# Optimization experiments

Hardware: AMD Instinct MI355X
Metric: run time of the kernel (lower is better)

The kernel has to match this reference:

```python
import jax, jax.numpy as jnp
import numpy as np

NUM_NODES = 8192
NUM_EDGES = 262144
IN_C = 512
OUT_C = 512


def setup_inputs() -> dict:
    key = jax.random.key(0)
    k1, k2, k3, k4 = jax.random.split(key, 4)
    x = jax.random.normal(k1, (NUM_NODES, IN_C), dtype=jnp.float32)
    edge_index = jax.random.randint(k2, (2, NUM_EDGES), 0, NUM_NODES, dtype=jnp.int64)
    # nn.Linear params (W: [out, in], b: [out]) with kaiming-ish scale
    W = jax.random.normal(k3, (OUT_C, IN_C), dtype=jnp.float32) * (1.0 / np.sqrt(IN_C))
    b = jax.random.normal(k4, (OUT_C,), dtype=jnp.float32) * 0.01
    return {"x": x, "edge_index": edge_index, "W": W, "b": b}


def reference(x, edge_index, W, b):
    n = x.shape[0]
    # append self loops
    loop = jnp.arange(n, dtype=edge_index.dtype)
    rows = jnp.concatenate([edge_index[0], loop])
    cols = jnp.concatenate([edge_index[1], loop])
    # dense adjacency via scatter-set (duplicates collapse to 1.0, matching torch indexing assign)
    adj = jnp.zeros((n, n), dtype=jnp.float32).at[rows, cols].set(1.0)
    deg = adj.sum(axis=1)
    deg_inv_sqrt = jnp.where(deg > 0, jax.lax.rsqrt(jnp.maximum(deg, 1e-30)), 0.0)
    norm = deg_inv_sqrt[:, None] * adj * deg_inv_sqrt[None, :]
    h = x @ W.T + b            # [N, out_c]
    return norm @ h            # [N, out_c]
```

## Files before the change

### kernel.cpp

```cpp
#include <hip/hip_runtime.h>
#include <stdint.h>

#define N_NODES 8192
#define N_EDGES 262144
#define IN_C    512
#define OUT_C   512
#define MAX_DEG 128
#define X_ELEMS (N_NODES * IN_C)
#define W_ELEMS (OUT_C * IN_C)
#define BM_WORDS (N_NODES * (N_NODES / 32))

typedef __attribute__((ext_vector_type(8))) short short8;
typedef __attribute__((ext_vector_type(4))) float f32x4;

__device__ inline uint16_t f2bf(float f) {
    uint32_t u = __float_as_uint(f);
    uint32_t r = (u + 0x7FFFu + ((u >> 16) & 1u)) >> 16;
    return (uint16_t)r;
}

__global__ __launch_bounds__(256) void convert_k(const float* __restrict__ x,
                                                 const float* __restrict__ W,
                                                 uint16_t* __restrict__ xb,
                                                 uint16_t* __restrict__ wb,
                                                 int* __restrict__ cnt,
                                                 uint4* __restrict__ bm) {
    int tid = blockIdx.x * 256 + threadIdx.x;
    if (tid < N_NODES) cnt[tid] = 0;
    if (tid < BM_WORDS / 4) bm[tid] = make_uint4(0u, 0u, 0u, 0u);
    int i = tid * 8;
    const float* src; uint16_t* dst;
    if (i < X_ELEMS) { src = x + i; dst = xb + i; }
    else             { src = W + (i - X_ELEMS); dst = wb + (i - X_ELEMS); }
    float4 v0 = *(const float4*)(src);
    float4 v1 = *(const float4*)(src + 4);
    ushort4 o0, o1;
    o0.x = f2bf(v0.x); o0.y = f2bf(v0.y); o0.z = f2bf(v0.z); o0.w = f2bf(v0.w);
    o1.x = f2bf(v1.x); o1.y = f2bf(v1.y); o1.z = f2bf(v1.z); o1.w = f2bf(v1.w);
    *(ushort4*)(dst)     = o0;
    *(ushort4*)(dst + 4) = o1;
}

__global__ __launch_bounds__(256) void gemm_scatter_k(const uint16_t* __restrict__ xb,
                                                      const uint16_t* __restrict__ wb,
                                                      const float* __restrict__ bias,
                                                      uint16_t* __restrict__ h,
                                                      const int* __restrict__ ei,
                                                      int* __restrict__ cnt,
                                                      uint16_t* __restrict__ nbr,
                                                      uint32_t* __restrict__ bm) {
    const int bid = blockIdx.x;
    if (bid < 256) {
        const int wave = threadIdx.x >> 6;
        const int lane = threadIdx.x & 63;
        const int quad = lane >> 4;
        const int l16  = lane & 15;
        const int mrow = (bid & 7) * 8 + (bid >> 5);
        const int ncol = (bid >> 3) & 3;
        const int m_base = mrow * 128 + (wave & 1) * 64;
        const int n_base = ncol * 128 + (wave >> 1) * 64;

        f32x4 acc[4][4];
        #pragma unroll
        for (int a = 0; a < 4; a++)
            #pragma unroll
            for (int s = 0; s < 4; s++) acc[a][s] = (f32x4){0.f, 0.f, 0.f, 0.f};

        #pragma unroll 2
        for (int k0 = 0; k0 < IN_C; k0 += 32) {
            short8 af[4], bf[4];
            #pragma unroll
            for (int a = 0; a < 4; a++)
                af[a] = *(const short8*)(xb + (m_base + a * 16 + l16) * IN_C + quad * 8 + k0);
            #pragma unroll
            for (int s = 0; s < 4; s++)
                bf[s] = *(const short8*)(wb + (n_base + s * 16 + l16) * IN_C + quad * 8 + k0);
            #pragma unroll
            for (int a = 0; a < 4; a++)
                #pragma unroll
                for (int s = 0; s < 4; s++)
                    acc[a][s] = __builtin_amdgcn_mfma_f32_16x16x32_bf16(bf[s], af[a], acc[a][s], 0, 0, 0);
        }
        #pragma unroll
        for (int s = 0; s < 4; s++) {
            int col_n0 = n_base + s * 16 + quad * 4;
            float4 bv = *(const float4*)(bias + col_n0);
            #pragma unroll
            for (int a = 0; a < 4; a++) {
                int row_m = m_base + a * 16 + l16;
                ushort4 o;
                o.x = f2bf(acc[a][s][0] + bv.x);
                o.y = f2bf(acc[a][s][1] + bv.y);
                o.z = f2bf(acc[a][s][2] + bv.z);
                o.w = f2bf(acc[a][s][3] + bv.w);
                *(ushort4*)(h + row_m * OUT_C + col_n0) = o;
            }
        }
    } else {
        int t = (bid - 256) * 256 + threadIdx.x;
        int r, c;
        if (t < N_EDGES) {
            r = ei[t];
            c = ei[N_EDGES + t];
        } else if (t < N_EDGES + N_NODES) {
            r = t - N_EDGES; c = r;
        } else return;
        uint32_t w   = (uint32_t)r * (uint32_t)(N_NODES / 32) + ((uint32_t)c >> 5);
        uint32_t bit = 1u << (c & 31);
        uint32_t old = atomicOr(&bm[w], bit);
        if (!(old & bit)) {
            int pos = atomicAdd(&cnt[r], 1);
            if (pos < MAX_DEG) nbr[r * MAX_DEG + pos] = (uint16_t)c;
        }
    }
}

__global__ __launch_bounds__(64) void aggregate_k(const int* __restrict__ cnt,
                                                  const uint16_t* __restrict__ nbr,
                                                  const uint32_t* __restrict__ h2,
                                                  float* __restrict__ out) {
    const int i    = blockIdx.x >> 2;
    const int q    = blockIdx.x & 3;
    const int lane = threadIdx.x;
    int m = cnt[i]; if (m > MAX_DEG) m = MAX_DEG;

    __shared__ uint16_t jl[MAX_DEG];
    __shared__ float    dl[MAX_DEG];
    for (int t = lane; t < m; t += 64) {
        uint16_t j = nbr[i * MAX_DEG + t];
        jl[t] = j;
        dl[t] = rsqrtf((float)cnt[j]);
    }
    __syncthreads();

    const uint32_t* hp = h2 + q * 64 + lane;
    float s0 = 0.f, s1 = 0.f;
    #pragma unroll 8
    for (int l = 0; l < m; l++) {
        uint32_t u = hp[(int)jl[l] * 256];
        float dj = dl[l];
        s0 += dj * __uint_as_float(u << 16);
        s1 += dj * __uint_as_float(u & 0xFFFF0000u);
    }
    float di = rsqrtf((float)m);
    int c = q * 128 + lane * 2;
    float2 o = {di * s0, di * s1};
    *(float2*)(out + i * OUT_C + c) = o;
}

extern "C" void kernel_launch(void* const* d_in, const int* in_sizes, int n_in,
                              void* d_out, int out_size, void* d_ws, size_t ws_size,
                              hipStream_t stream) {
    const float* x  = (const float*)d_in[0];
    const int*   ei = (const int*)  d_in[1];
    const float* W  = (const float*)d_in[2];
    const float* b  = (const float*)d_in[3];
    float* out = (float*)d_out;
    char* ws = (char*)d_ws;

    const size_t CNT_OFF = 0;
    const size_t BM_OFF  = 32768;
    const size_t NBR_OFF = BM_OFF + 8388608;
    const size_t XB_OFF  = NBR_OFF + 2097152;
    const size_t WB_OFF  = XB_OFF + 8388608;
    const size_t H_OFF   = WB_OFF + 524288;
    int*      cnt = (int*)     (ws + CNT_OFF);
    uint32_t* bm  = (uint32_t*)(ws + BM_OFF);
    uint16_t* nbr = (uint16_t*)(ws + NBR_OFF);
    uint16_t* xb  = (uint16_t*)(ws + XB_OFF);
    uint16_t* wb  = (uint16_t*)(ws + WB_OFF);
    uint16_t* h   = (uint16_t*)(ws + H_OFF);

    convert_k<<<(X_ELEMS + W_ELEMS) / (256 * 8), 256, 0, stream>>>(x, W, xb, wb, cnt, (uint4*)bm);

    gemm_scatter_k<<<256 + (N_EDGES + N_NODES + 255) / 256, 256, 0, stream>>>(
        xb, wb, b, h, ei, cnt, nbr, bm);

    aggregate_k<<<N_NODES * 4, 64, 0, stream>>>(cnt, nbr, (const uint32_t*)h, out);
}
```

Baseline: 126.9 us.

## Stage GEMM A/B tiles in LDS via global_load_lds for block-level reuse

The GEMM part previously had each wave load its A and B fragments straight from global memory, so tiles shared between waves were fetched more than once. It now loads 128x64 bf16 tiles of A and B into shared memory with direct global-to-LDS loads, syncs, and reads the MFMA fragments from LDS. This cuts global traffic and redundant loads but adds two barriers per k-step and has no double buffering. It also adds 32KB of LDS, which the edge-scatter blocks of the same kernel must reserve too, lowering their occupancy. The LDS rows are unpadded, so fragment reads may hit bank conflicts.

```diff
diff --git a/kernel.cpp b/kernel.cpp
--- a/kernel.cpp
+++ b/kernel.cpp
@@ -18,6 +18,11 @@
     uint32_t r = (u + 0x7FFFu + ((u >> 16) & 1u)) >> 16;
     return (uint16_t)r;
 }
+
+#define GLOAD_LDS16(g, l)                                                        \
+    __builtin_amdgcn_global_load_lds(                                            \
+        (const __attribute__((address_space(1))) uint32_t*)(g),                  \
+        (__attribute__((address_space(3))) uint32_t*)(l), 16, 0, 0)
 
 __global__ __launch_bounds__(256) void convert_k(const float* __restrict__ x,
                                                  const float* __restrict__ W,
@@ -49,6 +54,8 @@
                                                       int* __restrict__ cnt,
                                                       uint16_t* __restrict__ nbr,
                                                       uint32_t* __restrict__ bm) {
+    __shared__ uint16_t lA[128 * 64];
+    __shared__ uint16_t lB[128 * 64];
     const int bid = blockIdx.x;
     if (bid < 256) {
         const int wave = threadIdx.x >> 6;
@@ -57,8 +64,15 @@
         const int l16  = lane & 15;
         const int mrow = (bid & 7) * 8 + (bid >> 5);
         const int ncol = (bid >> 3) & 3;
-        const int m_base = mrow * 128 + (wave & 1) * 64;
-        const int n_base = ncol * 128 + (wave >> 1) * 64;
+        const int m0 = mrow * 128;
+        const int n0 = ncol * 128;
+        const int wm = wave & 1;
+        const int wn = wave >> 1;
+
+        const int srow = wave * 32 + (lane >> 3);
+        const int scol = (lane & 7) * 8;
+        uint16_t* lAdst = &lA[wave * 32 * 64];
+        uint16_t* lBdst = &lB[wave * 32 * 64];
 
         f32x4 acc[4][4];
         #pragma unroll
@@ -66,21 +80,32 @@
             #pragma unroll
             for (int s = 0; s < 4; s++) acc[a][s] = (f32x4){0.f, 0.f, 0.f, 0.f};
 
-        #pragma unroll 2
-        for (int k0 = 0; k0 < IN_C; k0 += 32) {
-            short8 af[4], bf[4];
-            #pragma unroll
-            for (int a = 0; a < 4; a++)
-                af[a] = *(const short8*)(xb + (m_base + a * 16 + l16) * IN_C + quad * 8 + k0);
-            #pragma unroll
-            for (int s = 0; s < 4; s++)
-                bf[s] = *(const short8*)(wb + (n_base + s * 16 + l16) * IN_C + quad * 8 + k0);
-            #pragma unroll
-            for (int a = 0; a < 4; a++)
+        for (int k0 = 0; k0 < IN_C; k0 += 64) {
+            #pragma unroll
+            for (int it = 0; it < 4; it++) {
+                GLOAD_LDS16(xb + (m0 + srow + it * 8) * IN_C + k0 + scol, lAdst + it * 8 * 64);
+                GLOAD_LDS16(wb + (n0 + srow + it * 8) * IN_C + k0 + scol, lBdst + it * 8 * 64);
+            }
+            __syncthreads();
+            #pragma unroll
+            for (int kk = 0; kk < 2; kk++) {
+                short8 af[4], bfr[4];
+                #pragma unroll
+                for (int a = 0; a < 4; a++)
+                    af[a] = *(const short8*)&lA[(wm * 64 + a * 16 + l16) * 64 + kk * 32 + quad * 8];
                 #pragma unroll
                 for (int s = 0; s < 4; s++)
-                    acc[a][s] = __builtin_amdgcn_mfma_f32_16x16x32_bf16(bf[s], af[a], acc[a][s], 0, 0, 0);
+                    bfr[s] = *(const short8*)&lB[(wn * 64 + s * 16 + l16) * 64 + kk * 32 + quad * 8];
+                #pragma unroll
+                for (int a = 0; a < 4; a++)
+                    #pragma unroll
+                    for (int s = 0; s < 4; s++)
+                        acc[a][s] = __builtin_amdgcn_mfma_f32_16x16x32_bf16(bfr[s], af[a], acc[a][s], 0, 0, 0);
+            }
+            __syncthreads();
         }
+        const int m_base = m0 + wm * 64;
+        const int n_base = n0 + wn * 64;
         #pragma unroll
         for (int s = 0; s < 4; s++) {
             int col_n0 = n_base + s * 16 + quad * 4;
```

Result: faster. 122.5 us (-3.5%).
